# Optimization experiments

Hardware: AMD Instinct MI355X
Metric: run time of the kernel (lower is better)

Reference implementation:

```python
import jax, jax.numpy as jnp
import numpy as np

EPS = 1e-5
K = 3
N_TAP = K * K


def _bn(x, g, b, m, v):
    # eval-mode batchnorm over channel axis 1 of NCHW
    inv = g / jnp.sqrt(v + EPS)
    return x * inv[None, :, None, None] + (b - m * inv)[None, :, None, None]


def _silu(x):
    return x * jax.nn.sigmoid(x)


def _dcn(x, offset, mask, w, b, pad=1):
    """Modulated deformable conv (DCNv2), stride 1.
    x: [B,C,H,W], offset: [B,2n,H,W] ((dy,dx) per tap), mask: [B,n,H,W],
    w: [O,C,K,K], b: [O]."""
    B, C, H, W = x.shape
    O = w.shape[0]
    ky, kx = jnp.meshgrid(jnp.arange(K), jnp.arange(K), indexing='ij')
    ky = ky.reshape(N_TAP).astype(x.dtype)
    kx = kx.reshape(N_TAP).astype(x.dtype)
    off = offset.reshape(B, N_TAP, 2, H, W)
    base_y = jnp.arange(H, dtype=x.dtype)[None, None, :, None]
    base_x = jnp.arange(W, dtype=x.dtype)[None, None, None, :]
    # fractional sample positions [B,n,H,W]
    py = base_y - pad + ky[None, :, None, None] + off[:, :, 0]
    px = base_x - pad + kx[None, :, None, None] + off[:, :, 1]
    y0 = jnp.floor(py)
    x0 = jnp.floor(px)
    fy = py - y0
    fx = px - x0
    y0i = y0.astype(jnp.int32)
    x0i = x0.astype(jnp.int32)
    x_flat = x.reshape(B, C, 1, H * W)

    def corner(yi, xi, wgt):
        valid = (yi >= 0) & (yi < H) & (xi >= 0) & (xi < W)
        idx = (jnp.clip(yi, 0, H - 1) * W + jnp.clip(xi, 0, W - 1)).reshape(B, 1, N_TAP, H * W)
        v = jnp.take_along_axis(x_flat, idx, axis=-1)  # [B,C,n,HW]
        return v * (wgt * valid.astype(x.dtype)).reshape(B, 1, N_TAP, H * W)

    acc = corner(y0i, x0i, (1 - fy) * (1 - fx))
    acc = acc + corner(y0i, x0i + 1, (1 - fy) * fx)
    acc = acc + corner(y0i + 1, x0i, fy * (1 - fx))
    acc = acc + corner(y0i + 1, x0i + 1, fy * fx)
    val = acc.reshape(B, C, N_TAP, H, W) * mask[:, None]  # modulation
    out = jnp.einsum('bcnhw,ocn->bohw', val, w.reshape(O, C, N_TAP))
    return out + b[None, :, None, None]


def setup_inputs() -> dict:
    key = jax.random.key(0)
    ks = jax.random.split(key, 16)
    B, C1, H, W = 8, 256, 80, 80
    C2 = 256
    Ch = 128  # c_ = int(c2 * 0.5)
    d = {}
    d['x'] = jax.random.normal(ks[0], (B, C1, H, W), jnp.float32)
    # cv1: 1x1 conv (no bias) + BN
    d['cv1_w'] = jax.random.normal(ks[1], (Ch, C1), jnp.float32) * (1.0 / np.sqrt(C1))
    d['bn1_g'] = jax.random.uniform(ks[2], (Ch,), jnp.float32, 0.5, 1.5)
    d['bn1_b'] = jax.random.normal(ks[3], (Ch,), jnp.float32) * 0.1
    d['bn1_m'] = jax.random.normal(ks[4], (Ch,), jnp.float32) * 0.1
    d['bn1_v'] = jax.random.uniform(ks[5], (Ch,), jnp.float32, 0.5, 1.5)
    # offset/mask predictor 3x3 conv (small weights -> modest deformation)
    d['off_w'] = jax.random.normal(ks[6], (3 * N_TAP, Ch, K, K), jnp.float32) * 0.01
    d['off_b'] = jnp.zeros((3 * N_TAP,), jnp.float32)
    # dcn main weight/bias
    d['dcn_w'] = jax.random.normal(ks[7], (Ch, Ch, K, K), jnp.float32) * (1.0 / np.sqrt(Ch * N_TAP))
    d['dcn_b'] = jnp.zeros((Ch,), jnp.float32)
    d['bn2_g'] = jax.random.uniform(ks[8], (Ch,), jnp.float32, 0.5, 1.5)
    d['bn2_b'] = jax.random.normal(ks[9], (Ch,), jnp.float32) * 0.1
    d['bn2_m'] = jax.random.normal(ks[10], (Ch,), jnp.float32) * 0.1
    d['bn2_v'] = jax.random.uniform(ks[11], (Ch,), jnp.float32, 0.5, 1.5)
    # cv2: 1x1 conv (no bias) + BN
    d['cv2_w'] = jax.random.normal(ks[12], (C2, Ch), jnp.float32) * (1.0 / np.sqrt(Ch))
    d['bn3_g'] = jax.random.uniform(ks[13], (C2,), jnp.float32, 0.5, 1.5)
    d['bn3_b'] = jax.random.normal(ks[14], (C2,), jnp.float32) * 0.1
    d['bn3_m'] = jax.random.normal(ks[15], (C2,), jnp.float32) * 0.1
    d['bn3_v'] = jnp.ones((C2,), jnp.float32)
    return d


def reference(x, cv1_w, bn1_g, bn1_b, bn1_m, bn1_v,
              off_w, off_b, dcn_w, dcn_b, bn2_g, bn2_b, bn2_m, bn2_v,
              cv2_w, bn3_g, bn3_b, bn3_m, bn3_v):
    # cv1: 1x1 conv -> BN -> SiLU
    y = _silu(_bn(jnp.einsum('bchw,oc->bohw', x, cv1_w), bn1_g, bn1_b, bn1_m, bn1_v))
    # offset/mask predictor: 3x3 conv, pad 1
    raw = jax.lax.conv_general_dilated(
        y, off_w, window_strides=(1, 1), padding=((1, 1), (1, 1)),
        dimension_numbers=('NCHW', 'OIHW', 'NCHW')) + off_b[None, :, None, None]
    offset = raw[:, :2 * N_TAP]
    mask = jax.nn.sigmoid(raw[:, 2 * N_TAP:])
    # modulated deformable 3x3 conv -> BN -> SiLU
    y = _silu(_bn(_dcn(y, offset, mask, dcn_w, dcn_b), bn2_g, bn2_b, bn2_m, bn2_v))
    # cv2: 1x1 conv -> BN -> SiLU
    y = _silu(_bn(jnp.einsum('bchw,oc->bohw', y, cv2_w), bn3_g, bn3_b, bn3_m, bn3_v))
    return x + y  # shortcut (c1 == c2)
```

## Files before the change

### kernel.cpp

```cpp
#include <hip/hip_runtime.h>
#include <math.h>

#define HWSZ 6400
#define WIMG 80
#define HIMG 80
#define BEPS 1e-5f

typedef __attribute__((ext_vector_type(8))) short short8;
typedef __attribute__((ext_vector_type(4))) float f32x4;
typedef __attribute__((ext_vector_type(4))) unsigned u32x4;

__device__ __forceinline__ unsigned short f2b(float f) {
    unsigned u = __builtin_bit_cast(unsigned, f);
    u += 0x7fffu + ((u >> 16) & 1u);
    return (unsigned short)(u >> 16);
}
__device__ __forceinline__ float silu_f(float t) { return t / (1.f + __expf(-t)); }

#define BMFMA(a, b, c) __builtin_amdgcn_mfma_f32_16x16x32_bf16(a, b, c, 0, 0, 0)

__device__ __forceinline__ void gload16(const unsigned short* g, unsigned short* l) {
    __builtin_amdgcn_global_load_lds(
        (const __attribute__((address_space(1))) unsigned int*)g,
        (__attribute__((address_space(3))) unsigned int*)l, 16, 0, 0);
}

__global__ __launch_bounds__(256) void k_prep(
    const float* __restrict__ cv1w, const float* __restrict__ g1, const float* __restrict__ b1,
    const float* __restrict__ m1, const float* __restrict__ v1,
    const float* __restrict__ offw, const float* __restrict__ offb,
    const float* __restrict__ dcnw, const float* __restrict__ dcnb,
    const float* __restrict__ g2, const float* __restrict__ b2,
    const float* __restrict__ m2, const float* __restrict__ v2,
    const float* __restrict__ cv2w, const float* __restrict__ g3, const float* __restrict__ b3,
    const float* __restrict__ m3, const float* __restrict__ v3,
    unsigned short* __restrict__ apk1, unsigned short* __restrict__ apko,
    unsigned short* __restrict__ apkd, unsigned short* __restrict__ apk2,
    float* __restrict__ bias1, float* __restrict__ biaso,
    float* __restrict__ bias2, float* __restrict__ bias3)
{
    int idx = blockIdx.x * 256 + threadIdx.x;
    if (idx < 32768) {
        int j = idx & 7, L = (idx >> 3) & 63, ks = (idx >> 9) & 7, mt = idx >> 12;
        int o = mt * 16 + (L & 15), k = ks * 32 + (L >> 4) * 8 + j;
        float inv = g1[o] * rsqrtf(v1[o] + BEPS);
        apk1[idx] = f2b(cv1w[o * 256 + k] * inv);
    } else if (idx < 69632) {
        int t = idx - 32768;
        int j = t & 7, L = (t >> 3) & 63;
        int mt = t / 18432, rem = t % 18432, ks = rem >> 9;
        int o = mt * 16 + (L & 15);
        int kp = ks * 32 + (L >> 4) * 8 + j;
        int n = kp >> 7, c = kp & 127;
        float wv = (o < 27) ? offw[(size_t)(o * 128 + c) * 9 + n] : 0.f;
        apko[((size_t)(ks * 2 + mt) * 64 + L) * 8 + j] = f2b(wv);
    } else if (idx < 217088) {
        int t = idx - 69632;
        int j = t & 7, L = (t >> 3) & 63;
        int mt = t / 18432, rem = t % 18432, ks = rem >> 9;
        int o = mt * 16 + (L & 15);
        int kp = ks * 32 + (L >> 4) * 8 + j;
        int n = kp >> 7, c = kp & 127;
        float inv = g2[o] * rsqrtf(v2[o] + BEPS);
        apkd[((size_t)(ks * 8 + mt) * 64 + L) * 8 + j] = f2b(dcnw[(size_t)(o * 128 + c) * 9 + n] * inv);
    } else if (idx < 249856) {
        int t = idx - 217088;
        int j = t & 7, L = (t >> 3) & 63, ks = (t >> 9) & 3, mt = t >> 11;
        int o = mt * 16 + (L & 15), k = ks * 32 + (L >> 4) * 8 + j;
        float inv = g3[o] * rsqrtf(v3[o] + BEPS);
        apk2[((size_t)(ks * 16 + mt) * 64 + L) * 8 + j] = f2b(cv2w[o * 128 + k] * inv);
    } else if (idx < 250395) {
        int t = idx - 249856;
        if (t < 128) { float inv = g1[t] * rsqrtf(v1[t] + BEPS); bias1[t] = b1[t] - m1[t] * inv; }
        else if (t < 155) { biaso[t - 128] = offb[t - 128]; }
        else if (t < 283) { int o = t - 155; float inv = g2[o] * rsqrtf(v2[o] + BEPS);
                            bias2[o] = dcnb[o] * inv + b2[o] - m2[o] * inv; }
        else { int o = t - 283; float inv = g3[o] * rsqrtf(v3[o] + BEPS); bias3[o] = b3[o] - m3[o] * inv; }
    }
}

__global__ __launch_bounds__(256) void k_cv1(
    const float* __restrict__ x, const unsigned short* __restrict__ apk1,
    const float* __restrict__ bias1, unsigned short* __restrict__ y1t)
{
    __shared__ __align__(16) unsigned short sB[20480];
    int blk = blockIdx.x;
    int b = blk / 100, pt = blk % 100;
    int p0 = pt * 64;
    int tid = threadIdx.x;
    int lane = tid & 63;
    int w = tid >> 6;
    {
        int px = lane, q = w;
        const float* xb = x + (size_t)b * 256 * HWSZ + p0 + px;
        for (int ks = 0; ks < 8; ++ks) {
            unsigned pk[4];
#pragma unroll
            for (int t = 0; t < 4; ++t) {
                float f0 = xb[(size_t)(ks * 32 + q * 8 + 2 * t) * HWSZ];
                float f1 = xb[(size_t)(ks * 32 + q * 8 + 2 * t + 1) * HWSZ];
                asm("v_cvt_pk_bf16_f32 %0, %1, %2" : "=v"(pk[t]) : "v"(f0), "v"(f1));
            }
            *(u32x4*)&sB[((ks * 4 + (px >> 4)) * 16 + (px & 15)) * 40 + q * 8] =
                (u32x4){pk[0], pk[1], pk[2], pk[3]};
        }
    }
    __syncthreads();
    int n16 = lane & 15, qd = lane >> 4;
    f32x4 acc[2][4];
#pragma unroll
    for (int mi = 0; mi < 2; ++mi)
#pragma unroll
        for (int nt = 0; nt < 4; ++nt) acc[mi][nt] = (f32x4){0.f, 0.f, 0.f, 0.f};
#pragma unroll
    for (int ks = 0; ks < 8; ++ks) {
        short8 a0 = *(const short8*)&apk1[(size_t)(((w * 2 + 0) * 8 + ks) * 64 + lane) * 8];
        short8 a1 = *(const short8*)&apk1[(size_t)(((w * 2 + 1) * 8 + ks) * 64 + lane) * 8];
        short8 bf[4];
#pragma unroll
        for (int nt = 0; nt < 4; ++nt)
            bf[nt] = *(const short8*)&sB[((ks * 4 + nt) * 16 + n16) * 40 + qd * 8];
#pragma unroll
        for (int nt = 0; nt < 4; ++nt) acc[0][nt] = BMFMA(a0, bf[nt], acc[0][nt]);
#pragma unroll
        for (int nt = 0; nt < 4; ++nt) acc[1][nt] = BMFMA(a1, bf[nt], acc[1][nt]);
    }
    __syncthreads();
#pragma unroll
    for (int mi = 0; mi < 2; ++mi)
#pragma unroll
        for (int nt = 0; nt < 4; ++nt)
#pragma unroll
            for (int r = 0; r < 4; ++r) {
                int o = w * 32 + mi * 16 + qd * 4 + r;
                float sv = silu_f(acc[mi][nt][r] + bias1[o]);
                sB[(nt * 16 + n16) * 136 + o] = f2b(sv);
            }
    __syncthreads();
    {
        int px = tid >> 2, qq = tid & 3;
        unsigned short* ytb = y1t + ((size_t)b * HWSZ + p0 + px) * 128;
#pragma unroll
        for (int seg = 0; seg < 4; ++seg) {
            short8 v = *(const short8*)&sB[px * 136 + qq * 32 + seg * 8];
            *(short8*)&ytb[qq * 32 + seg * 8] = v;
        }
    }
}

#define NSLAB 53

#define ACC8(uu, cb)                                                                   \
    {                                                                                  \
        _Pragma("unroll") for (int t = 0; t < 4; ++t) {                                \
            unsigned uv = (uu)[t];                                                     \
            av[(cb) + 2 * t] = fmaf(wk, __builtin_bit_cast(float, uv << 16),           \
                                    av[(cb) + 2 * t]);                                 \
            av[(cb) + 2 * t + 1] = fmaf(wk, __builtin_bit_cast(float, uv & 0xffff0000u),\
                                        av[(cb) + 2 * t + 1]);                         \
        }                                                                              \
    }

__device__ __forceinline__ const unsigned short* slab_src(
    const unsigned short* apko, const unsigned short* apkd,
    const unsigned short* apk2, int i) {
    if (i < 9)  return apko + (size_t)i * 4096;
    if (i < 45) return apkd + (size_t)(i - 9) * 4096;
    return apk2 + (size_t)(i - 45) * 4096;
}

#define STAGE(i, bp)                                                                   \
    {                                                                                  \
        const unsigned short* src_ = slab_src(apko, apkd, apk2, (i));                  \
        gload16(src_ + ((w * 2 + 0) * 512 + lane * 8), &sAf[bp][(w * 2 + 0) * 512]);   \
        gload16(src_ + ((w * 2 + 1) * 512 + lane * 8), &sAf[bp][(w * 2 + 1) * 512]);   \
    }

__global__ __launch_bounds__(256, 4) void k_odc(
    const unsigned short* __restrict__ y1t,
    const unsigned short* __restrict__ apko, const float* __restrict__ biaso,
    const unsigned short* __restrict__ apkd, const float* __restrict__ bias2,
    const unsigned short* __restrict__ apk2, const float* __restrict__ bias3,
    const float* __restrict__ x, float* __restrict__ out)
{
    __shared__ float sRaw[27 * 66];
    __shared__ __align__(16) unsigned short sAf[2][4096];
    __shared__ __align__(16) unsigned short sZ[64 * 132];

    int blk = blockIdx.x;
    int b = blk / 100, pt = blk % 100;
    int h0 = (pt / 5) * 4, w0 = (pt % 5) * 16;
    int tid = threadIdx.x, lane = tid & 63, w = tid >> 6;
    int n16 = lane & 15, qd = lane >> 4;
    int pxl = w * 16 + n16;
    const unsigned short* yb = y1t + (size_t)b * HWSZ * 128;

    STAGE(0, 0)
    __syncthreads();
    int bufp = 0;

    {
        f32x4 oa0 = (f32x4){0.f, 0.f, 0.f, 0.f};
        f32x4 oa1 = (f32x4){0.f, 0.f, 0.f, 0.f};
        for (int n = 0; n < 9; ++n) {
            STAGE(n + 1, bufp ^ 1)
            int dh = n / 3 - 1, dw = n % 3 - 1;
            int hh = h0 + w + dh, ww = w0 + n16 + dw;
            bool valid = ((unsigned)hh < HIMG) && ((unsigned)ww < WIMG);
            int row = min(max(hh, 0), HIMG - 1) * WIMG + min(max(ww, 0), WIMG - 1);
            const unsigned short* ys = &yb[(size_t)row * 128 + qd * 8];
            short8 bfv[4];
#pragma unroll
            for (int s = 0; s < 4; ++s) {
                short8 v = *(const short8*)&ys[s * 32];
                if (!valid) v = (short8){0, 0, 0, 0, 0, 0, 0, 0};
                bfv[s] = v;
            }
#pragma unroll
            for (int s = 0; s < 4; ++s) {
                short8 a0 = *(const short8*)&sAf[bufp][(s * 2 + 0) * 512 + lane * 8];
                short8 a1 = *(const short8*)&sAf[bufp][(s * 2 + 1) * 512 + lane * 8];
                oa0 = BMFMA(a0, bfv[s], oa0);
                oa1 = BMFMA(a1, bfv[s], oa1);
            }
            if (n == 8) {
#pragma unroll
                for (int mi = 0; mi < 2; ++mi)
#pragma unroll
                    for (int r4 = 0; r4 < 4; ++r4) {
                        int o = mi * 16 + qd * 4 + r4;
                        if (o < 27) {
                            float t = (mi ? oa1[r4] : oa0[r4]) + biaso[o];
                            if (o >= 18) t = 1.f / (1.f + __expf(-t));
                            sRaw[o * 66 + pxl] = t;
                        }
                    }
            }
            __syncthreads();
            bufp ^= 1;
        }
    }

    f32x4 acc[8];
#pragma unroll
    for (int mt = 0; mt < 8; ++mt) acc[mt] = (f32x4){0.f, 0.f, 0.f, 0.f};
    int hI = h0 + w, wI = w0 + n16;

    for (int n = 0; n < 9; ++n) {
        float av[32];
#pragma unroll
        for (int s = 0; s < 4; ++s) {
            int slab = 9 + n * 4 + s;
            if (slab + 1 < NSLAB) STAGE(slab + 1, bufp ^ 1)
            if (s == 0) {
                float dy = sRaw[(2 * n) * 66 + pxl];
                float dx = sRaw[(2 * n + 1) * 66 + pxl];
                float mk = sRaw[(18 + n) * 66 + pxl];
                float py = (float)(hI - 1 + n / 3) + dy;
                float px = (float)(wI - 1 + n % 3) + dx;
                float y0f = floorf(py), x0f = floorf(px);
                float fy = py - y0f, fxv = px - x0f;
                int y0 = (int)y0f, x0 = (int)x0f;
                float wy0 = (1.f - fy) * mk, wy1 = fy * mk, fx1 = 1.f - fxv;
#pragma unroll
                for (int j = 0; j < 32; ++j) av[j] = 0.f;
#pragma unroll
                for (int k = 0; k < 4; ++k) {
                    int yy = y0 + (k >> 1), xx = x0 + (k & 1);
                    bool vld = ((unsigned)yy < HIMG) && ((unsigned)xx < WIMG);
                    float wk = ((k >> 1) ? wy1 : wy0) * ((k & 1) ? fxv : fx1);
                    if (!vld) wk = 0.f;
                    int yc = min(max(yy, 0), HIMG - 1);
                    int xc = min(max(xx, 0), WIMG - 1);
                    const unsigned short* src = &yb[(size_t)(yc * WIMG + xc) * 128 + qd * 8];
                    u32x4 u0 = *(const u32x4*)src;
                    u32x4 u1 = *(const u32x4*)(src + 32);
                    u32x4 u2 = *(const u32x4*)(src + 64);
                    u32x4 u3 = *(const u32x4*)(src + 96);
                    ACC8(u0, 0) ACC8(u1, 8) ACC8(u2, 16) ACC8(u3, 24)
                }
            }
            unsigned pk0, pk1, pk2, pk3;
            asm("v_cvt_pk_bf16_f32 %0, %1, %2" : "=v"(pk0) : "v"(av[s * 8 + 0]), "v"(av[s * 8 + 1]));
            asm("v_cvt_pk_bf16_f32 %0, %1, %2" : "=v"(pk1) : "v"(av[s * 8 + 2]), "v"(av[s * 8 + 3]));
            asm("v_cvt_pk_bf16_f32 %0, %1, %2" : "=v"(pk2) : "v"(av[s * 8 + 4]), "v"(av[s * 8 + 5]));
            asm("v_cvt_pk_bf16_f32 %0, %1, %2" : "=v"(pk3) : "v"(av[s * 8 + 6]), "v"(av[s * 8 + 7]));
            short8 bfv = __builtin_bit_cast(short8, (u32x4){pk0, pk1, pk2, pk3});
#pragma unroll
            for (int mt = 0; mt < 8; ++mt) {
                short8 af = *(const short8*)&sAf[bufp][mt * 512 + lane * 8];
                acc[mt] = BMFMA(af, bfv, acc[mt]);
            }
            if (n == 8 && s == 3) {
#pragma unroll
                for (int mt = 0; mt < 8; ++mt)
#pragma unroll
                    for (int r4 = 0; r4 < 4; ++r4) {
                        int o = mt * 16 + qd * 4 + r4;
                        float sv = silu_f(acc[mt][r4] + bias2[o]);
                        sZ[pxl * 132 + o] = f2b(sv);
                    }
            }
            __syncthreads();
            bufp ^= 1;
        }
    }

    f32x4 c2[16];
#pragma unroll
    for (int mt = 0; mt < 16; ++mt) c2[mt] = (f32x4){0.f, 0.f, 0.f, 0.f};
#pragma unroll
    for (int h2 = 0; h2 < 8; ++h2) {
        int slab = 45 + h2;
        if (slab + 1 < NSLAB) STAGE(slab + 1, bufp ^ 1)
        int ks = h2 >> 1, half = h2 & 1;
        short8 bf = *(const short8*)&sZ[pxl * 132 + ks * 32 + qd * 8];
#pragma unroll
        for (int mt = 0; mt < 8; ++mt) {
            short8 af = *(const short8*)&sAf[bufp][mt * 512 + lane * 8];
            c2[half * 8 + mt] = BMFMA(af, bf, c2[half * 8 + mt]);
        }
        __syncthreads();
        bufp ^= 1;
    }
    int p = (h0 + w) * WIMG + w0 + n16;
    const float* xb = x + (size_t)b * 256 * HWSZ;
    float* ob = out + (size_t)b * 256 * HWSZ;
#pragma unroll
    for (int mt = 0; mt < 16; ++mt)
#pragma unroll
        for (int r4 = 0; r4 < 4; ++r4) {
            int o = mt * 16 + qd * 4 + r4;
            size_t idx = (size_t)o * HWSZ + p;
            ob[idx] = xb[idx] + silu_f(c2[mt][r4] + bias3[o]);
        }
}

extern "C" void kernel_launch(void* const* d_in, const int* in_sizes, int n_in,
                              void* d_out, int out_size, void* d_ws, size_t ws_size,
                              hipStream_t stream) {
    const float* x     = (const float*)d_in[0];
    const float* cv1w  = (const float*)d_in[1];
    const float* bn1g  = (const float*)d_in[2];
    const float* bn1b  = (const float*)d_in[3];
    const float* bn1m  = (const float*)d_in[4];
    const float* bn1v  = (const float*)d_in[5];
    const float* offw  = (const float*)d_in[6];
    const float* offb  = (const float*)d_in[7];
    const float* dcnw  = (const float*)d_in[8];
    const float* dcnb  = (const float*)d_in[9];
    const float* bn2g  = (const float*)d_in[10];
    const float* bn2b  = (const float*)d_in[11];
    const float* bn2m  = (const float*)d_in[12];
    const float* bn2v  = (const float*)d_in[13];
    const float* cv2w  = (const float*)d_in[14];
    const float* bn3g  = (const float*)d_in[15];
    const float* bn3b  = (const float*)d_in[16];
    const float* bn3m  = (const float*)d_in[17];
    const float* bn3v  = (const float*)d_in[18];
    float* out = (float*)d_out;

    float* base = (float*)d_ws;
    unsigned short* y1t = (unsigned short*)base;
    unsigned short* apk1 = (unsigned short*)(base + 7936000);
    unsigned short* apko = (unsigned short*)(base + 7952384);
    unsigned short* apkd = (unsigned short*)(base + 7970816);
    unsigned short* apk2 = (unsigned short*)(base + 8044544);
    float* bias1 = base + 8060928;
    float* biaso = base + 8061056;
    float* bias2 = base + 8061088;
    float* bias3 = base + 8061216;

    k_prep<<<979, 256, 0, stream>>>(cv1w, bn1g, bn1b, bn1m, bn1v,
                                    offw, offb, dcnw, dcnb,
                                    bn2g, bn2b, bn2m, bn2v,
                                    cv2w, bn3g, bn3b, bn3m, bn3v,
                                    apk1, apko, apkd, apk2,
                                    bias1, biaso, bias2, bias3);
    k_cv1<<<800, 256, 0, stream>>>(x, apk1, bias1, y1t);
    k_odc<<<800, 256, 0, stream>>>(y1t, apko, biaso, apkd, bias2,
                                   apk2, bias3, x, out);
}
```

Before: 248.0 us.

## Deepen weight-slab prefetch to two ahead with explicit vmcnt waits

The fused offset/DCN/cv2 kernel now issues the weight-slab global-to-LDS load two slabs ahead instead of one. Each step waits on vmcnt(2) using split barriers, replacing a full __syncthreads that drained all outstanding loads. The cv1 kernel hoists its A-fragment loads out of the MFMA loop and packs x to bf16 through a software round instead of v_cvt_pk. The aim is to hide global latency behind MFMA work, at the cost of extra barriers and hand-tuned waitcnt logic that could be fragile.

```diff
diff --git a/kernel.cpp b/kernel.cpp
--- a/kernel.cpp
+++ b/kernel.cpp
@@ -90,19 +90,21 @@
     int tid = threadIdx.x;
     int lane = tid & 63;
     int w = tid >> 6;
+    short8 af0[8], af1[8];
+#pragma unroll
+    for (int ks = 0; ks < 8; ++ks) {
+        af0[ks] = *(const short8*)&apk1[(size_t)(((w * 2 + 0) * 8 + ks) * 64 + lane) * 8];
+        af1[ks] = *(const short8*)&apk1[(size_t)(((w * 2 + 1) * 8 + ks) * 64 + lane) * 8];
+    }
     {
         int px = lane, q = w;
         const float* xb = x + (size_t)b * 256 * HWSZ + p0 + px;
         for (int ks = 0; ks < 8; ++ks) {
-            unsigned pk[4];
-#pragma unroll
-            for (int t = 0; t < 4; ++t) {
-                float f0 = xb[(size_t)(ks * 32 + q * 8 + 2 * t) * HWSZ];
-                float f1 = xb[(size_t)(ks * 32 + q * 8 + 2 * t + 1) * HWSZ];
-                asm("v_cvt_pk_bf16_f32 %0, %1, %2" : "=v"(pk[t]) : "v"(f0), "v"(f1));
-            }
-            *(u32x4*)&sB[((ks * 4 + (px >> 4)) * 16 + (px & 15)) * 40 + q * 8] =
-                (u32x4){pk[0], pk[1], pk[2], pk[3]};
+            short8 v;
+#pragma unroll
+            for (int j = 0; j < 8; ++j)
+                v[j] = (short)f2b(xb[(size_t)(ks * 32 + q * 8 + j) * HWSZ]);
+            *(short8*)&sB[((ks * 4 + (px >> 4)) * 16 + (px & 15)) * 40 + q * 8] = v;
         }
     }
     __syncthreads();
@@ -114,16 +116,14 @@
         for (int nt = 0; nt < 4; ++nt) acc[mi][nt] = (f32x4){0.f, 0.f, 0.f, 0.f};
 #pragma unroll
     for (int ks = 0; ks < 8; ++ks) {
-        short8 a0 = *(const short8*)&apk1[(size_t)(((w * 2 + 0) * 8 + ks) * 64 + lane) * 8];
-        short8 a1 = *(const short8*)&apk1[(size_t)(((w * 2 + 1) * 8 + ks) * 64 + lane) * 8];
         short8 bf[4];
 #pragma unroll
         for (int nt = 0; nt < 4; ++nt)
             bf[nt] = *(const short8*)&sB[((ks * 4 + nt) * 16 + n16) * 40 + qd * 8];
 #pragma unroll
-        for (int nt = 0; nt < 4; ++nt) acc[0][nt] = BMFMA(a0, bf[nt], acc[0][nt]);
-#pragma unroll
-        for (int nt = 0; nt < 4; ++nt) acc[1][nt] = BMFMA(a1, bf[nt], acc[1][nt]);
+        for (int nt = 0; nt < 4; ++nt) acc[0][nt] = BMFMA(af0[ks], bf[nt], acc[0][nt]);
+#pragma unroll
+        for (int nt = 0; nt < 4; ++nt) acc[1][nt] = BMFMA(af1[ks], bf[nt], acc[1][nt]);
     }
     __syncthreads();
 #pragma unroll
@@ -174,6 +174,23 @@
         const unsigned short* src_ = slab_src(apko, apkd, apk2, (i));                  \
         gload16(src_ + ((w * 2 + 0) * 512 + lane * 8), &sAf[bp][(w * 2 + 0) * 512]);   \
         gload16(src_ + ((w * 2 + 1) * 512 + lane * 8), &sAf[bp][(w * 2 + 1) * 512]);   \
+    }
+
+#define SLAB_SYNC(slab)                                                                \
+    {                                                                                  \
+        asm volatile("s_waitcnt lgkmcnt(0)" ::: "memory");                             \
+        __builtin_amdgcn_sched_barrier(0);                                             \
+        __builtin_amdgcn_s_barrier();                                                  \
+        if ((slab) + 2 < NSLAB) {                                                      \
+            STAGE((slab) + 2, bufp)                                                    \
+            asm volatile("s_waitcnt vmcnt(2)" ::: "memory");                           \
+        } else {                                                                       \
+            asm volatile("s_waitcnt vmcnt(0)" ::: "memory");                           \
+        }                                                                              \
+        __builtin_amdgcn_sched_barrier(0);                                             \
+        __builtin_amdgcn_s_barrier();                                                  \
+        __builtin_amdgcn_sched_barrier(0);                                             \
+        bufp ^= 1;                                                                     \
     }
 
 __global__ __launch_bounds__(256, 4) void k_odc(
@@ -196,14 +213,17 @@
     const unsigned short* yb = y1t + (size_t)b * HWSZ * 128;
 
     STAGE(0, 0)
-    __syncthreads();
+    STAGE(1, 1)
+    asm volatile("s_waitcnt vmcnt(2)" ::: "memory");
+    __builtin_amdgcn_sched_barrier(0);
+    __builtin_amdgcn_s_barrier();
+    __builtin_amdgcn_sched_barrier(0);
     int bufp = 0;
 
     {
         f32x4 oa0 = (f32x4){0.f, 0.f, 0.f, 0.f};
         f32x4 oa1 = (f32x4){0.f, 0.f, 0.f, 0.f};
         for (int n = 0; n < 9; ++n) {
-            STAGE(n + 1, bufp ^ 1)
             int dh = n / 3 - 1, dw = n % 3 - 1;
             int hh = h0 + w + dh, ww = w0 + n16 + dw;
             bool valid = ((unsigned)hh < HIMG) && ((unsigned)ww < WIMG);
@@ -236,8 +256,7 @@
                         }
                     }
             }
-            __syncthreads();
-            bufp ^= 1;
+            SLAB_SYNC(n)
         }
     }
 
@@ -251,7 +270,6 @@
 #pragma unroll
         for (int s = 0; s < 4; ++s) {
             int slab = 9 + n * 4 + s;
-            if (slab + 1 < NSLAB) STAGE(slab + 1, bufp ^ 1)
             if (s == 0) {
                 float dy = sRaw[(2 * n) * 66 + pxl];
                 float dx = sRaw[(2 * n + 1) * 66 + pxl];
@@ -301,8 +319,7 @@
                         sZ[pxl * 132 + o] = f2b(sv);
                     }
             }
-            __syncthreads();
-            bufp ^= 1;
+            SLAB_SYNC(slab)
         }
     }
 
@@ -312,7 +329,6 @@
 #pragma unroll
     for (int h2 = 0; h2 < 8; ++h2) {
         int slab = 45 + h2;
-        if (slab + 1 < NSLAB) STAGE(slab + 1, bufp ^ 1)
         int ks = h2 >> 1, half = h2 & 1;
         short8 bf = *(const short8*)&sZ[pxl * 132 + ks * 32 + qd * 8];
 #pragma unroll
@@ -320,8 +336,7 @@
             short8 af = *(const short8*)&sAf[bufp][mt * 512 + lane * 8];
             c2[half * 8 + mt] = BMFMA(af, bf, c2[half * 8 + mt]);
         }
-        __syncthreads();
-        bufp ^= 1;
+        SLAB_SYNC(slab)
     }
     int p = (h0 + w) * WIMG + w0 + n16;
     const float* xb = x + (size_t)b * 256 * HWSZ;
```

New measurement: 248.6 us. Within noise of the previous version (+0.3%).
